# Kernel tuning notes

Measured on AMD Instinct MI355X. Metric: run time of the kernel, lower is better.

The kernel has to match this reference:

```python
import jax, jax.numpy as jnp
import numpy as np

B, D, F, H = 256, 9, 8, 256   # batch of trees, tree depth, input features, hidden
N = 2 ** (D + 1) - 1          # total nodes per full binary tree (heap layout)


def _init(key, shape, fan_in):
    return jax.random.normal(key, shape, jnp.float32) * (1.0 / np.sqrt(fan_in))


def setup_inputs() -> dict:
    key = jax.random.key(0)
    ks = jax.random.split(key, 6)
    return {
        "data": jax.random.normal(ks[0], (B, N, F), jnp.float32),
        "Wu": _init(ks[1], (H, F), F),
        "bu": jnp.zeros((H,), jnp.float32),
        "Wr": _init(ks[2], (3 * H, 3 * H), 3 * H),
        "br": jnp.zeros((3 * H,), jnp.float32),
        "Wh": _init(ks[3], (H, 3 * H), 3 * H),
        "bh": jnp.zeros((H,), jnp.float32),
        "Wz": _init(ks[4], (4 * H, 4 * H), 4 * H),
        "bz": jnp.zeros((4 * H,), jnp.float32),
        "Wp": _init(ks[5], (1, H), H),
        "bp": jnp.zeros((1,), jnp.float32),
    }


def reference(data, Wu, bu, Wr, br, Wh, bh, Wz, bz, Wp, bp):
    # data: [B, N, F] node features in heap (level-order) layout;
    # children of the i-th node of level l are nodes 2i, 2i+1 of level l+1.
    b, n_nodes, _ = data.shape
    L = (n_nodes + 1) // 2          # number of leaves
    depth = L.bit_length() - 1
    h_dim = Wu.shape[0]

    # leaf embedding u for every node (leaf() is applied at every tree node)
    u = jnp.einsum('bnf,hf->bnh', data, Wu) + bu          # [B, N, H]
    h = u[:, L - 1:, :]                                    # leaf level states [B, L, H]

    for l in range(depth - 1, -1, -1):                     # bottom-up over levels
        n = 2 ** l
        parent = u[:, n - 1:2 * n - 1, :]                  # [B, n, H]
        h_l, h_r = h[:, 0::2, :], h[:, 1::2, :]            # [B, n, H] each
        hhu = jnp.concatenate([parent, h_l, h_r], axis=-1)  # [B, n, 3H]
        r = jax.nn.sigmoid(jnp.einsum('bnk,jk->bnj', hhu, Wr) + br)
        h_new = jax.nn.relu(jnp.einsum('bnk,hk->bnh', r * hhu, Wh) + bh)
        hhhu = jnp.concatenate([h_new, hhu], axis=-1)      # [B, n, 4H]
        zlin = jnp.einsum('bnk,jk->bnj', hhhu, Wz) + bz    # [B, n, 4H]
        z = jax.nn.softmax(zlin.reshape(b, n, 4, h_dim), axis=2)
        h = (z * hhhu.reshape(b, n, 4, h_dim)).sum(axis=2)  # gated combine -> [B, n, H]

    # h is [B, 1, H] at the root; logits head
    logits = jnp.einsum('bnh,oh->bno', h, Wp) + bp          # [B, 1, 1]
    return logits[:, 0, 0]                                  # [B]
```

## Files before the change

### kernel.cpp

```cpp
#include <hip/hip_runtime.h>
#include <math.h>

#define BB 256
#define NN 1023
#define FF 8
#define HH 256
#define DEPTH 9

enum { EPI_NONE = 0, EPI_SIGMUL = 1, EPI_RELU = 2, EPI_COMBINE = 3 };

typedef __bf16 bf16x8_t __attribute__((ext_vector_type(8)));
typedef __bf16 bf16x4_t __attribute__((ext_vector_type(4)));
typedef float f32x4_t __attribute__((ext_vector_type(4)));

__device__ __forceinline__ void stage16(const void* g, void* l) {
    __builtin_amdgcn_global_load_lds(
        (const __attribute__((address_space(1))) void*)g,
        (__attribute__((address_space(3))) void*)l,
        16, 0, 0);
}

template <int EPI>
__global__ __launch_bounds__(512) void gemm256(
    const __bf16* __restrict__ A, int lda,
    const __bf16* __restrict__ W,
    const float* __restrict__ bias,
    const __bf16* __restrict__ aux, int ldaux,
    void* __restrict__ Cout, int ldc,
    int K)
{
    __shared__ __bf16 lds[2][2][256 * 64];
    const int tid = threadIdx.x;
    const int lane = tid & 63;
    const int w = tid >> 6;
    const int wr = w >> 2, wc = w & 3;

    const int nwg = gridDim.x * gridDim.y;
    const int hw = blockIdx.y * gridDim.x + blockIdx.x;
    const int xcd = hw & 7, k0 = hw >> 3;
    const int qq = nwg >> 3, rr = nwg & 7;
    const int wg = (xcd < rr ? xcd * (qq + 1) : rr * (qq + 1) + (xcd - rr) * qq) + k0;
    const int bm0 = (wg / gridDim.x) * 256;
    const int bn0 = (wg % gridDim.x) * 256;

    const int srow = tid >> 3;
    const int scol = (tid & 7) * 8;

    f32x4_t acc[8][4];
#pragma unroll
    for (int i = 0; i < 8; ++i)
#pragma unroll
        for (int j = 0; j < 4; ++j) acc[i][j] = (f32x4_t){0.f, 0.f, 0.f, 0.f};

    const int rA = lane & 15;
    const int klane = (lane >> 4) * 8;
    const int NT = K >> 6;

#pragma unroll
    for (int p = 0; p < 4; ++p) {
        stage16(A + (size_t)(bm0 + p * 64 + srow) * lda + scol,
                &lds[0][0][p * 4096 + w * 512]);
        stage16(W + (size_t)(bn0 + p * 64 + srow) * K + scol,
                &lds[0][1][p * 4096 + w * 512]);
    }
    __syncthreads();

    for (int kt = 0; kt < NT; ++kt) {
        const int cur = kt & 1;
        if (kt + 1 < NT) {
            const int kk = (kt + 1) << 6;
#pragma unroll
            for (int p = 0; p < 4; ++p) {
                stage16(A + (size_t)(bm0 + p * 64 + srow) * lda + kk + scol,
                        &lds[cur ^ 1][0][p * 4096 + w * 512]);
                stage16(W + (size_t)(bn0 + p * 64 + srow) * K + kk + scol,
                        &lds[cur ^ 1][1][p * 4096 + w * 512]);
            }
        }
        const __bf16* As = lds[cur][0];
        const __bf16* Bs = lds[cur][1];
#pragma unroll
        for (int ks = 0; ks < 2; ++ks) {
            bf16x8_t af[8], bfr[4];
#pragma unroll
            for (int i = 0; i < 8; ++i)
                af[i] = *(const bf16x8_t*)&As[(wr * 128 + i * 16 + rA) * 64 + ks * 32 + klane];
#pragma unroll
            for (int j = 0; j < 4; ++j)
                bfr[j] = *(const bf16x8_t*)&Bs[(wc * 64 + j * 16 + rA) * 64 + ks * 32 + klane];
#pragma unroll
            for (int i = 0; i < 8; ++i)
#pragma unroll
                for (int j = 0; j < 4; ++j)
                    acc[i][j] = __builtin_amdgcn_mfma_f32_16x16x32_bf16(
                        af[i], bfr[j], acc[i][j], 0, 0, 0);
        }
        __syncthreads();
    }

    if (EPI == EPI_COMBINE) {
        const int r = lane & 15;
        const int G = ((bn0 + wc * 64) >> 2) + r;
        float bz4[4];
#pragma unroll
        for (int g = 0; g < 4; ++g) bz4[g] = bias[bn0 + wc * 64 + g * 16 + r];
#pragma unroll
        for (int i = 0; i < 8; ++i) {
#pragma unroll
            for (int reg = 0; reg < 4; ++reg) {
                const int gr = bm0 + wr * 128 + i * 16 + (lane >> 4) * 4 + reg;
                float z0 = acc[i][0][reg] + bz4[0];
                float z1 = acc[i][1][reg] + bz4[1];
                float z2 = acc[i][2][reg] + bz4[2];
                float z3 = acc[i][3][reg] + bz4[3];
                float mx = fmaxf(fmaxf(z0, z1), fmaxf(z2, z3));
                float e0 = __expf(z0 - mx), e1 = __expf(z1 - mx);
                float e2 = __expf(z2 - mx), e3 = __expf(z3 - mx);
                const __bf16* hrow = aux + (size_t)gr * ldaux + G;
                float hv = (e0 * (float)hrow[0] + e1 * (float)hrow[256] +
                            e2 * (float)hrow[512] + e3 * (float)hrow[768]) /
                           (e0 + e1 + e2 + e3);
                ((__bf16*)Cout)[(size_t)gr * ldc + G] = (__bf16)hv;
            }
        }
    } else {
#pragma unroll
        for (int j = 0; j < 4; ++j) {
            const int gc = bn0 + wc * 64 + j * 16 + (lane & 15);
            const float bv = bias[gc];
#pragma unroll
            for (int i = 0; i < 8; ++i) {
#pragma unroll
                for (int reg = 0; reg < 4; ++reg) {
                    const int gr = bm0 + wr * 128 + i * 16 + (lane >> 4) * 4 + reg;
                    float v = acc[i][j][reg] + bv;
                    if (EPI == EPI_SIGMUL) {
                        float s = 1.0f / (1.0f + __expf(-v));
                        v = s * (float)aux[(size_t)gr * ldaux + gc];
                        ((__bf16*)Cout)[(size_t)gr * ldc + gc] = (__bf16)v;
                    } else if (EPI == EPI_RELU) {
                        v = fmaxf(v, 0.0f);
                        ((__bf16*)Cout)[(size_t)gr * ldc + gc] = (__bf16)v;
                    } else {
                        ((float*)Cout)[(size_t)gr * ldc + gc] = v;
                    }
                }
            }
        }
    }
}

template <int EPI>
__global__ __launch_bounds__(256) void gemm_mfma(
    const __bf16* __restrict__ A, int lda,
    const __bf16* __restrict__ W,
    const float* __restrict__ bias,
    const __bf16* __restrict__ aux, int ldaux,
    void* __restrict__ Cout, int ldc,
    int K)
{
    __shared__ __bf16 As[128 * 32];
    __shared__ __bf16 Bs[128 * 32];
    const int tid = threadIdx.x;
    const int lane = tid & 63;
    const int w = tid >> 6;
    const int wr = w >> 1, wc = w & 1;

    const int nwg = gridDim.x * gridDim.y;
    const int hw = blockIdx.y * gridDim.x + blockIdx.x;
    const int xcd = hw & 7, k0 = hw >> 3;
    const int qq = nwg >> 3, rr = nwg & 7;
    const int wg = (xcd < rr ? xcd * (qq + 1) : rr * (qq + 1) + (xcd - rr) * qq) + k0;
    const int bm0 = (wg / gridDim.x) * 128;
    const int bn0 = (wg % gridDim.x) * 128;

    const int srow = lane >> 2;
    const int scol = (lane & 3) * 8;

    f32x4_t acc[4][4];
#pragma unroll
    for (int i = 0; i < 4; ++i)
#pragma unroll
        for (int j = 0; j < 4; ++j) acc[i][j] = (f32x4_t){0.f, 0.f, 0.f, 0.f};

    const int rA = lane & 15;
    const int kslot = (lane >> 4) * 8;

    for (int kk = 0; kk < K; kk += 32) {
        stage16(A + (size_t)(bm0 + w * 16 + srow) * lda + kk + scol,
                &As[(w * 16) * 32]);
        stage16(A + (size_t)(bm0 + 64 + w * 16 + srow) * lda + kk + scol,
                &As[(64 + w * 16) * 32]);
        stage16(W + (size_t)(bn0 + w * 16 + srow) * K + kk + scol,
                &Bs[(w * 16) * 32]);
        stage16(W + (size_t)(bn0 + 64 + w * 16 + srow) * K + kk + scol,
                &Bs[(64 + w * 16) * 32]);
        __syncthreads();

        bf16x8_t af[4], bfr[4];
#pragma unroll
        for (int i = 0; i < 4; ++i)
            af[i] = *(const bf16x8_t*)&As[(wr * 64 + i * 16 + rA) * 32 + kslot];
#pragma unroll
        for (int j = 0; j < 4; ++j)
            bfr[j] = *(const bf16x8_t*)&Bs[(wc * 64 + j * 16 + rA) * 32 + kslot];
#pragma unroll
        for (int i = 0; i < 4; ++i)
#pragma unroll
            for (int j = 0; j < 4; ++j)
                acc[i][j] = __builtin_amdgcn_mfma_f32_16x16x32_bf16(
                    af[i], bfr[j], acc[i][j], 0, 0, 0);
        __syncthreads();
    }

    if (EPI == EPI_COMBINE) {
        const int r = lane & 15;
        const int G = ((bn0 + wc * 64) >> 2) + r;
        float bz4[4];
#pragma unroll
        for (int g = 0; g < 4; ++g) bz4[g] = bias[bn0 + wc * 64 + g * 16 + r];
#pragma unroll
        for (int i = 0; i < 4; ++i) {
#pragma unroll
            for (int reg = 0; reg < 4; ++reg) {
                const int gr = bm0 + wr * 64 + i * 16 + (lane >> 4) * 4 + reg;
                float z0 = acc[i][0][reg] + bz4[0];
                float z1 = acc[i][1][reg] + bz4[1];
                float z2 = acc[i][2][reg] + bz4[2];
                float z3 = acc[i][3][reg] + bz4[3];
                float mx = fmaxf(fmaxf(z0, z1), fmaxf(z2, z3));
                float e0 = __expf(z0 - mx), e1 = __expf(z1 - mx);
                float e2 = __expf(z2 - mx), e3 = __expf(z3 - mx);
                const __bf16* hrow = aux + (size_t)gr * ldaux + G;
                float hv = (e0 * (float)hrow[0] + e1 * (float)hrow[256] +
                            e2 * (float)hrow[512] + e3 * (float)hrow[768]) /
                           (e0 + e1 + e2 + e3);
                ((__bf16*)Cout)[(size_t)gr * ldc + G] = (__bf16)hv;
            }
        }
    } else {
#pragma unroll
        for (int j = 0; j < 4; ++j) {
            const int gc = bn0 + wc * 64 + j * 16 + (lane & 15);
            const float bv = bias[gc];
#pragma unroll
            for (int i = 0; i < 4; ++i) {
#pragma unroll
                for (int reg = 0; reg < 4; ++reg) {
                    const int gr = bm0 + wr * 64 + i * 16 + (lane >> 4) * 4 + reg;
                    float v = acc[i][j][reg] + bv;
                    if (EPI == EPI_SIGMUL) {
                        float s = 1.0f / (1.0f + __expf(-v));
                        v = s * (float)aux[(size_t)gr * ldaux + gc];
                        ((__bf16*)Cout)[(size_t)gr * ldc + gc] = (__bf16)v;
                    } else if (EPI == EPI_RELU) {
                        v = fmaxf(v, 0.0f);
                        ((__bf16*)Cout)[(size_t)gr * ldc + gc] = (__bf16)v;
                    } else {
                        ((float*)Cout)[(size_t)gr * ldc + gc] = v;
                    }
                }
            }
        }
    }
}

__global__ __launch_bounds__(256) void convert_weights(
    const float* __restrict__ Wr, const float* __restrict__ Wh,
    const float* __restrict__ Wz, const float* __restrict__ bz,
    __bf16* __restrict__ Wrb, __bf16* __restrict__ Whb,
    __bf16* __restrict__ Wzb, float* __restrict__ bzp)
{
    const int NR = 768 * 768, NH2 = 256 * 768, NZ = 1024 * 1024;
    const int idx0 = blockIdx.x * 256 + threadIdx.x;
    for (int i = idx0; i < NR + NH2 + NZ; i += gridDim.x * 256) {
        if (i < NR) Wrb[i] = (__bf16)Wr[i];
        else if (i < NR + NH2) Whb[i - NR] = (__bf16)Wh[i - NR];
        else {
            const int z = i - NR - NH2;
            const int p = z >> 10, k = z & 1023;
            const int o = ((p >> 4) & 3) * 256 + (p >> 6) * 16 + (p & 15);
            Wzb[z] = (__bf16)Wz[(size_t)o * 1024 + k];
        }
    }
    if (idx0 < 1024) {
        const int p = idx0;
        const int o = ((p >> 4) & 3) * 256 + (p >> 6) * 16 + (p & 15);
        bzp[p] = bz[o];
    }
}

__global__ __launch_bounds__(256) void build_hhu(
    const float* __restrict__ data, const float* __restrict__ Wu,
    const float* __restrict__ bu, const __bf16* __restrict__ hprev,
    __bf16* __restrict__ hhhu, int l, int r0)
{
    const int n = 1 << l;
    const int row = blockIdx.x * 8 + (threadIdx.x >> 5);
    const int c0 = (threadIdx.x & 31) * 8;
    const int i = r0 + row;
    const int b = i >> l;
    const int m = i & (n - 1);

    float wv[8][8];
#pragma unroll
    for (int cc = 0; cc < 8; ++cc) {
        float4 w0 = *(const float4*)&Wu[(c0 + cc) * 8];
        float4 w1 = *(const float4*)&Wu[(c0 + cc) * 8 + 4];
        wv[cc][0] = w0.x; wv[cc][1] = w0.y; wv[cc][2] = w0.z; wv[cc][3] = w0.w;
        wv[cc][4] = w1.x; wv[cc][5] = w1.y; wv[cc][6] = w1.z; wv[cc][7] = w1.w;
    }
    float buv[8];
#pragma unroll
    for (int cc = 0; cc < 8; ++cc) buv[cc] = bu[c0 + cc];

    __bf16* rowp = hhhu + (size_t)row * 1024;

    {
        const float* dp = data + ((size_t)b * NN + (n - 1) + m) * FF;
        float4 d0 = *(const float4*)dp, d1 = *(const float4*)(dp + 4);
        float dv[8] = {d0.x, d0.y, d0.z, d0.w, d1.x, d1.y, d1.z, d1.w};
        bf16x8_t o;
#pragma unroll
        for (int cc = 0; cc < 8; ++cc) {
            float acc = buv[cc];
#pragma unroll
            for (int f = 0; f < 8; ++f) acc += dv[f] * wv[cc][f];
            o[cc] = (__bf16)acc;
        }
        *(bf16x8_t*)&rowp[256 + c0] = o;
    }

    if (l == 8) {
        const float* dl = data + ((size_t)b * NN + 511 + 2 * m) * FF;
#pragma unroll
        for (int side = 0; side < 2; ++side) {
            const float* dp = dl + side * FF;
            float4 d0 = *(const float4*)dp, d1 = *(const float4*)(dp + 4);
            float dv[8] = {d0.x, d0.y, d0.z, d0.w, d1.x, d1.y, d1.z, d1.w};
            bf16x8_t o;
#pragma unroll
            for (int cc = 0; cc < 8; ++cc) {
                float acc = buv[cc];
#pragma unroll
                for (int f = 0; f < 8; ++f) acc += dv[f] * wv[cc][f];
                o[cc] = (__bf16)acc;
            }
            *(bf16x8_t*)&rowp[512 + side * 256 + c0] = o;
        }
    } else {
        *(bf16x8_t*)&rowp[512 + c0] =
            *(const bf16x8_t*)&hprev[((size_t)b * (2 * n) + 2 * m) * HH + c0];
        *(bf16x8_t*)&rowp[768 + c0] =
            *(const bf16x8_t*)&hprev[((size_t)b * (2 * n) + 2 * m + 1) * HH + c0];
    }
}

__global__ __launch_bounds__(256) void final_kernel(
    const __bf16* __restrict__ hfin, const float* __restrict__ Wp,
    const float* __restrict__ bp, float* __restrict__ out)
{
    const int b = blockIdx.x;
    const int t = threadIdx.x;
    __shared__ float red[256];
    red[t] = (float)hfin[(size_t)b * HH + t] * Wp[t];
    __syncthreads();
    for (int s = 128; s > 0; s >>= 1) {
        if (t < s) red[t] += red[t + s];
        __syncthreads();
    }
    if (t == 0) out[b] = red[0] + bp[0];
}

extern "C" void kernel_launch(void* const* d_in, const int* in_sizes, int n_in,
                              void* d_out, int out_size, void* d_ws, size_t ws_size,
                              hipStream_t stream)
{
    const float* data = (const float*)d_in[0];
    const float* Wu = (const float*)d_in[1];
    const float* bu = (const float*)d_in[2];
    const float* Wr = (const float*)d_in[3];
    const float* br = (const float*)d_in[4];
    const float* Wh = (const float*)d_in[5];
    const float* bh = (const float*)d_in[6];
    const float* Wz = (const float*)d_in[7];
    const float* bz = (const float*)d_in[8];
    const float* Wp = (const float*)d_in[9];
    const float* bp = (const float*)d_in[10];
    float* out = (float*)d_out;

    const size_t CAP = 32768;
    char* w = (char*)d_ws;
    __bf16* hA = (__bf16*)w;   w += (size_t)65536 * HH * 2;
    __bf16* hB = (__bf16*)w;   w += (size_t)32768 * HH * 2;
    __bf16* hhhu = (__bf16*)w; w += CAP * 1024 * 2;
    __bf16* rh = (__bf16*)w;   w += CAP * 768 * 2;
    __bf16* Wrb = (__bf16*)w;  w += (size_t)768 * 768 * 2;
    __bf16* Whb = (__bf16*)w;  w += (size_t)256 * 768 * 2;
    __bf16* Wzb = (__bf16*)w;  w += (size_t)1024 * 1024 * 2;
    float* bzp = (float*)w;    w += 1024 * 4;

    convert_weights<<<2048, 256, 0, stream>>>(Wr, Wh, Wz, bz, Wrb, Whb, Wzb, bzp);

    for (int l = DEPTH - 1; l >= 0; --l) {
        const size_t M = (size_t)BB << l;
        __bf16* dst = ((DEPTH - 1 - l) & 1) ? hB : hA;
        const __bf16* src = ((DEPTH - 1 - l) & 1) ? hA : hB;
        for (size_t r0 = 0; r0 < M; r0 += CAP) {
            const int R = (int)((M - r0 < CAP) ? (M - r0) : CAP);
            build_hhu<<<R / 8, 256, 0, stream>>>(data, Wu, bu, src, hhhu, l, (int)r0);
            if (R >= 32768) {
                gemm256<EPI_SIGMUL><<<dim3(3, R / 256), 512, 0, stream>>>(
                    hhhu + 256, 1024, Wrb, br, hhhu + 256, 1024, rh, 768, 768);
            } else {
                gemm_mfma<EPI_SIGMUL><<<dim3(6, R / 128), 256, 0, stream>>>(
                    hhhu + 256, 1024, Wrb, br, hhhu + 256, 1024, rh, 768, 768);
            }
            gemm_mfma<EPI_RELU><<<dim3(2, R / 128), 256, 0, stream>>>(
                rh, 768, Whb, bh, nullptr, 0, hhhu, 1024, 768);
            if (R >= 16384) {
                gemm256<EPI_COMBINE><<<dim3(4, R / 256), 512, 0, stream>>>(
                    hhhu, 1024, Wzb, bzp, hhhu, 1024,
                    dst + (size_t)r0 * HH, HH, 1024);
            } else {
                gemm_mfma<EPI_COMBINE><<<dim3(8, R / 128), 256, 0, stream>>>(
                    hhhu, 1024, Wzb, bzp, hhhu, 1024,
                    dst + (size_t)r0 * HH, HH, 1024);
            }
        }
    }
    final_kernel<<<BB, 256, 0, stream>>>(hA, Wp, bp, out);
}
```

Before: 1.252 ms.

## Deepen 256x256 GEMM pipeline with XOR-swizzled LDS, interleaved MFMA, wider dispatch

Rewrites the 256-tile GEMM main loop to prefetch two K-tiles ahead, using explicit vmcnt waits and barriers with sched_barrier fences. MFMA issue is interleaved with LDS fragment loads, and s_setprio is raised during the final MFMA block. LDS is XOR-swizzled on both store and read to cut bank conflicts, and launch_bounds asks for 2 blocks per CU. The large-tile kernel now also runs for smaller row counts (R>=2048), which risks poorer occupancy and tail effects on the small levels, plus correctness risk from hand-written waitcnt counts.

Result: no change. 1.240 ms (-1.0%).

```diff
diff --git a/kernel.cpp b/kernel.cpp
--- a/kernel.cpp
+++ b/kernel.cpp
@@ -10,7 +10,6 @@
 enum { EPI_NONE = 0, EPI_SIGMUL = 1, EPI_RELU = 2, EPI_COMBINE = 3 };
 
 typedef __bf16 bf16x8_t __attribute__((ext_vector_type(8)));
-typedef __bf16 bf16x4_t __attribute__((ext_vector_type(4)));
 typedef float f32x4_t __attribute__((ext_vector_type(4)));
 
 __device__ __forceinline__ void stage16(const void* g, void* l) {
@@ -21,7 +20,7 @@
 }
 
 template <int EPI>
-__global__ __launch_bounds__(512) void gemm256(
+__global__ __launch_bounds__(512, 2) void gemm256p(
     const __bf16* __restrict__ A, int lda,
     const __bf16* __restrict__ W,
     const float* __restrict__ bias,
@@ -44,7 +43,7 @@
     const int bn0 = (wg % gridDim.x) * 256;
 
     const int srow = tid >> 3;
-    const int scol = (tid & 7) * 8;
+    const int scolz = ((tid & 7) ^ ((tid >> 3) & 7)) * 8;
 
     f32x4_t acc[8][4];
 #pragma unroll
@@ -54,49 +53,100 @@
 
     const int rA = lane & 15;
     const int klane = (lane >> 4) * 8;
+    const int rxor = (lane & 7) * 8;
     const int NT = K >> 6;
 
-#pragma unroll
-    for (int p = 0; p < 4; ++p) {
-        stage16(A + (size_t)(bm0 + p * 64 + srow) * lda + scol,
-                &lds[0][0][p * 4096 + w * 512]);
-        stage16(W + (size_t)(bn0 + p * 64 + srow) * K + scol,
-                &lds[0][1][p * 4096 + w * 512]);
-    }
-    __syncthreads();
-
-    for (int kt = 0; kt < NT; ++kt) {
-        const int cur = kt & 1;
-        if (kt + 1 < NT) {
-            const int kk = (kt + 1) << 6;
-#pragma unroll
-            for (int p = 0; p < 4; ++p) {
-                stage16(A + (size_t)(bm0 + p * 64 + srow) * lda + kk + scol,
-                        &lds[cur ^ 1][0][p * 4096 + w * 512]);
-                stage16(W + (size_t)(bn0 + p * 64 + srow) * K + kk + scol,
-                        &lds[cur ^ 1][1][p * 4096 + w * 512]);
-            }
-        }
-        const __bf16* As = lds[cur][0];
-        const __bf16* Bs = lds[cur][1];
-#pragma unroll
-        for (int ks = 0; ks < 2; ++ks) {
-            bf16x8_t af[8], bfr[4];
-#pragma unroll
-            for (int i = 0; i < 8; ++i)
-                af[i] = *(const bf16x8_t*)&As[(wr * 128 + i * 16 + rA) * 64 + ks * 32 + klane];
+#define STAGE_T(t, buf)                                                        \
+    do {                                                                       \
+        const int kk_ = (t) << 6;                                              \
+        _Pragma("unroll")                                                      \
+        for (int rnd = 0; rnd < 4; ++rnd) {                                    \
+            stage16(A + (size_t)(bm0 + rnd * 64 + srow) * lda + kk_ + scolz,   \
+                    &lds[buf][0][rnd * 4096 + w * 512]);                       \
+            stage16(W + (size_t)(bn0 + rnd * 64 + srow) * K + kk_ + scolz,     \
+                    &lds[buf][1][rnd * 4096 + w * 512]);                       \
+        }                                                                      \
+    } while (0)
+
+#define LDA_F(As_, i, ks) \
+    (*(const bf16x8_t*)&(As_)[(wr * 128 + (i) * 16 + rA) * 64 + (((ks) * 32 + klane) ^ rxor)])
+#define LDB_F(Bs_, j, ks) \
+    (*(const bf16x8_t*)&(Bs_)[(wc * 64 + (j) * 16 + rA) * 64 + (((ks) * 32 + klane) ^ rxor)])
+
+    STAGE_T(0, 0);
+    STAGE_T(1, 1);
+    asm volatile("s_waitcnt vmcnt(8)" ::: "memory");
+    __builtin_amdgcn_sched_barrier(0);
+    __builtin_amdgcn_s_barrier();
+    __builtin_amdgcn_sched_barrier(0);
+
+    for (int t = 0; t < NT; ++t) {
+        const int p = t & 1;
+        const __bf16* As = lds[p][0];
+        const __bf16* Bs = lds[p][1];
+
+        bf16x8_t b0[4], b1[4], alo[4], ahi[4];
+#pragma unroll
+        for (int j = 0; j < 4; ++j) b0[j] = LDB_F(Bs, j, 0);
+#pragma unroll
+        for (int i = 0; i < 4; ++i) alo[i] = LDA_F(As, i, 0);
+#pragma unroll
+        for (int i = 0; i < 4; ++i)
 #pragma unroll
             for (int j = 0; j < 4; ++j)
-                bfr[j] = *(const bf16x8_t*)&Bs[(wc * 64 + j * 16 + rA) * 64 + ks * 32 + klane];
-#pragma unroll
-            for (int i = 0; i < 8; ++i)
-#pragma unroll
-                for (int j = 0; j < 4; ++j)
-                    acc[i][j] = __builtin_amdgcn_mfma_f32_16x16x32_bf16(
-                        af[i], bfr[j], acc[i][j], 0, 0, 0);
-        }
-        __syncthreads();
-    }
+                acc[i][j] = __builtin_amdgcn_mfma_f32_16x16x32_bf16(
+                    alo[i], b0[j], acc[i][j], 0, 0, 0);
+#pragma unroll
+        for (int i = 0; i < 4; ++i) ahi[i] = LDA_F(As, 4 + i, 0);
+#pragma unroll
+        for (int i = 0; i < 4; ++i)
+#pragma unroll
+            for (int j = 0; j < 4; ++j)
+                acc[4 + i][j] = __builtin_amdgcn_mfma_f32_16x16x32_bf16(
+                    ahi[i], b0[j], acc[4 + i][j], 0, 0, 0);
+#pragma unroll
+        for (int j = 0; j < 4; ++j) b1[j] = LDB_F(Bs, j, 1);
+#pragma unroll
+        for (int i = 0; i < 4; ++i) alo[i] = LDA_F(As, i, 1);
+#pragma unroll
+        for (int i = 0; i < 4; ++i) ahi[i] = LDA_F(As, 4 + i, 1);
+#pragma unroll
+        for (int i = 0; i < 4; ++i)
+#pragma unroll
+            for (int j = 0; j < 4; ++j)
+                acc[i][j] = __builtin_amdgcn_mfma_f32_16x16x32_bf16(
+                    alo[i], b1[j], acc[i][j], 0, 0, 0);
+
+        asm volatile("s_waitcnt lgkmcnt(0)" ::: "memory");
+        __builtin_amdgcn_sched_barrier(0);
+        __builtin_amdgcn_s_barrier();
+        __builtin_amdgcn_sched_barrier(0);
+
+        if (t + 2 < NT) STAGE_T(t + 2, p);
+
+        __builtin_amdgcn_s_setprio(1);
+#pragma unroll
+        for (int i = 0; i < 4; ++i)
+#pragma unroll
+            for (int j = 0; j < 4; ++j)
+                acc[4 + i][j] = __builtin_amdgcn_mfma_f32_16x16x32_bf16(
+                    ahi[i], b1[j], acc[4 + i][j], 0, 0, 0);
+        __builtin_amdgcn_s_setprio(0);
+
+        if (t + 1 < NT) {
+            if (t + 2 < NT) {
+                asm volatile("s_waitcnt vmcnt(8)" ::: "memory");
+            } else {
+                asm volatile("s_waitcnt vmcnt(0)" ::: "memory");
+            }
+            __builtin_amdgcn_sched_barrier(0);
+            __builtin_amdgcn_s_barrier();
+            __builtin_amdgcn_sched_barrier(0);
+        }
+    }
+#undef STAGE_T
+#undef LDA_F
+#undef LDB_F
 
     if (EPI == EPI_COMBINE) {
         const int r = lane & 15;
@@ -409,8 +459,8 @@
         for (size_t r0 = 0; r0 < M; r0 += CAP) {
             const int R = (int)((M - r0 < CAP) ? (M - r0) : CAP);
             build_hhu<<<R / 8, 256, 0, stream>>>(data, Wu, bu, src, hhhu, l, (int)r0);
-            if (R >= 32768) {
-                gemm256<EPI_SIGMUL><<<dim3(3, R / 256), 512, 0, stream>>>(
+            if (R >= 2048) {
+                gemm256p<EPI_SIGMUL><<<dim3(3, R / 256), 512, 0, stream>>>(
                     hhhu + 256, 1024, Wrb, br, hhhu + 256, 1024, rh, 768, 768);
             } else {
                 gemm_mfma<EPI_SIGMUL><<<dim3(6, R / 128), 256, 0, stream>>>(
@@ -418,8 +468,8 @@
             }
             gemm_mfma<EPI_RELU><<<dim3(2, R / 128), 256, 0, stream>>>(
                 rh, 768, Whb, bh, nullptr, 0, hhhu, 1024, 768);
-            if (R >= 16384) {
-                gemm256<EPI_COMBINE><<<dim3(4, R / 256), 512, 0, stream>>>(
+            if (R >= 2048) {
+                gemm256p<EPI_COMBINE><<<dim3(4, R / 256), 512, 0, stream>>>(
                     hhhu, 1024, Wzb, bzp, hhhu, 1024,
                     dst + (size_t)r0 * HH, HH, 1024);
             } else {
```
